# Kernel optimization log

Measured on AMD Instinct MI355X. Metric: run time of the kernel, lower is better.

Reference implementation:

```python
import jax, jax.numpy as jnp
import numpy as np

NUM_TASKS = 8
NUM_EXPERTS = 8
TOPK = 2
WEX = 0.01
N_TOKENS = 4194304


def setup_inputs() -> dict:
    key = jax.random.key(0)
    k1, k2 = jax.random.split(key)
    router_logits = jax.random.normal(k1, (N_TOKENS, NUM_EXPERTS), dtype=jnp.float32)
    router_labels = jax.random.randint(k2, (N_TOKENS,), 0, NUM_TASKS, dtype=jnp.int64)
    return {"router_logits": router_logits, "router_labels": router_labels}


def reference(router_logits, router_labels):
    # call_update: detached softmax over experts
    probs = jax.lax.stop_gradient(
        jax.nn.softmax(router_logits.astype(jnp.float32), axis=-1)
    )  # [N, E]
    labels = router_labels.astype(jnp.int32)
    # Torch loop `for task in router_labels` adds segment_sum[task] once per
    # occurrence of task -> EX_task_gate[t] = count[t] * segment_sum[t]
    seg_sum = jax.ops.segment_sum(probs, labels, num_segments=NUM_TASKS)  # [T, E]
    counts = jax.ops.segment_sum(
        jnp.ones((probs.shape[0],), dtype=jnp.float32), labels, num_segments=NUM_TASKS
    )  # [T]
    EX_gate = seg_sum * counts[:, None]  # [T, E]
    # calculate_mutual_information_loss
    tot = EX_gate.sum() / TOPK
    EX_gate = EX_gate / (tot + 0.0001)
    P_TI = EX_gate.sum(axis=1, keepdims=True) + 0.0001  # [T, 1]
    P_EI = EX_gate.sum(axis=0, keepdims=True) + 0.0001  # [1, E]
    expert_loss = -(EX_gate * jnp.log(EX_gate / P_TI / P_EI + 0.0001)).sum()
    return jnp.float32(WEX) * expert_loss
```

## Files before the change

### kernel.cpp

```cpp
#include <hip/hip_runtime.h>
#include <hip/hip_bf16.h>

#define N_TOKENS    4194304
#define NUM_EXPERTS 8
#define NUM_TASKS   8
#define GRID        2048
#define BLOCK       256
#define NTHREADS    (GRID * BLOCK)
#define ITERS       (N_TOKENS * 2 / NTHREADS)
#define BATCH       4

__global__ __launch_bounds__(BLOCK) void mi_reduce_kernel(
    const float* __restrict__ logits,
    const int*   __restrict__ labels,
    float*       __restrict__ ws) {

  float acc[NUM_TASKS][4];
#pragma unroll
  for (int t = 0; t < NUM_TASKS; ++t)
#pragma unroll
    for (int e = 0; e < 4; ++e) acc[t][e] = 0.0f;

  const int u    = blockIdx.x * BLOCK + threadIdx.x;
  const int tok0 = u >> 1;
  const float4* __restrict__ lp = reinterpret_cast<const float4*>(logits);

#pragma unroll
  for (int kb = 0; kb < ITERS / BATCH; ++kb) {
    float4 v[BATCH];
    int   lab[BATCH];
#pragma unroll
    for (int j = 0; j < BATCH; ++j) {
      const int k = kb * BATCH + j;
      v[j]   = lp[(size_t)k * NTHREADS + u];
      lab[j] = labels[k * (NTHREADS / 2) + tok0];
    }
#pragma unroll
    for (int j = 0; j < BATCH; ++j) {
      float mx = fmaxf(fmaxf(v[j].x, v[j].y), fmaxf(v[j].z, v[j].w));
      mx = fmaxf(mx, __shfl_xor(mx, 1, 64));
      float p0 = __expf(v[j].x - mx);
      float p1 = __expf(v[j].y - mx);
      float p2 = __expf(v[j].z - mx);
      float p3 = __expf(v[j].w - mx);
      float s = (p0 + p1) + (p2 + p3);
      s += __shfl_xor(s, 1, 64);
      float r = __builtin_amdgcn_rcpf(s);
      p0 *= r; p1 *= r; p2 *= r; p3 *= r;
#pragma unroll
      for (int t = 0; t < NUM_TASKS; ++t) {
        float m = (lab[j] == t) ? 1.0f : 0.0f;
        acc[t][0] = fmaf(m, p0, acc[t][0]);
        acc[t][1] = fmaf(m, p1, acc[t][1]);
        acc[t][2] = fmaf(m, p2, acc[t][2]);
        acc[t][3] = fmaf(m, p3, acc[t][3]);
      }
    }
  }

#pragma unroll
  for (int t = 0; t < NUM_TASKS; ++t)
#pragma unroll
    for (int e = 0; e < 4; ++e) {
      float x = acc[t][e];
#pragma unroll
      for (int m = 2; m < 64; m <<= 1) x += __shfl_xor(x, m, 64);
      acc[t][e] = x;
    }

  __shared__ float sacc[64];
  if (threadIdx.x < 64) sacc[threadIdx.x] = 0.0f;
  __syncthreads();
  const int lane = threadIdx.x & 63;
  if (lane < 2) {
    const int eoff = lane * 4;
#pragma unroll
    for (int t = 0; t < NUM_TASKS; ++t)
#pragma unroll
      for (int e = 0; e < 4; ++e)
        atomicAdd(&sacc[t * NUM_EXPERTS + eoff + e], acc[t][e]);
  }
  __syncthreads();
  if (threadIdx.x < 64) atomicAdd(&ws[threadIdx.x], sacc[threadIdx.x]);
}

__global__ void mi_finalize_kernel(const float* __restrict__ ws,
                                   float* __restrict__ out) {
  int lane = threadIdx.x;

  float seg = ws[lane];

  float c = seg;
  c += __shfl_xor(c, 1, 64);
  c += __shfl_xor(c, 2, 64);
  c += __shfl_xor(c, 4, 64);

  float ex = seg * c;

  float s = ex;
#pragma unroll
  for (int m = 1; m < 64; m <<= 1) s += __shfl_xor(s, m, 64);
  float tot = s * 0.5f;
  ex = ex / (tot + 1e-4f);

  float pti = ex;
  pti += __shfl_xor(pti, 1, 64);
  pti += __shfl_xor(pti, 2, 64);
  pti += __shfl_xor(pti, 4, 64);
  pti += 1e-4f;

  float pei = ex;
  pei += __shfl_xor(pei, 8, 64);
  pei += __shfl_xor(pei, 16, 64);
  pei += __shfl_xor(pei, 32, 64);
  pei += 1e-4f;

  float term = -ex * logf(ex / pti / pei + 1e-4f);
#pragma unroll
  for (int m = 1; m < 64; m <<= 1) term += __shfl_xor(term, m, 64);

  if (lane == 0) out[0] = 0.01f * term;
}

extern "C" void kernel_launch(void* const* d_in, const int* in_sizes, int n_in,
                              void* d_out, int out_size, void* d_ws, size_t ws_size,
                              hipStream_t stream) {
  const float* logits = (const float*)d_in[0];
  const int*   labels = (const int*)d_in[1];
  float* out = (float*)d_out;
  float* ws  = (float*)d_ws;

  hipMemsetAsync(ws, 0, 64 * sizeof(float), stream);

  mi_reduce_kernel<<<GRID, BLOCK, 0, stream>>>(logits, labels, ws);
  mi_finalize_kernel<<<1, 64, 0, stream>>>(ws, out);
}
```

Measured before the change: 232.8 us.

## Halve grid, double-buffer loads, replace global atomics with per-block partials

Halves the grid so each thread handles 32 token-halves, processed in four batches of 8. Loads are double-buffered so the next batch is in flight while the current one is reduced. The global atomicAdd and the memset are replaced by per-block partial writes, which a 1024-thread finalize kernel sums. This removes atomic contention and the memset launch, at the cost of higher register pressure and a larger finalize reduction.

```diff
diff --git a/kernel.cpp b/kernel.cpp
--- a/kernel.cpp
+++ b/kernel.cpp
@@ -4,16 +4,16 @@
 #define N_TOKENS    4194304
 #define NUM_EXPERTS 8
 #define NUM_TASKS   8
-#define GRID        2048
+#define GRID        1024
 #define BLOCK       256
-#define NTHREADS    (GRID * BLOCK)
-#define ITERS       (N_TOKENS * 2 / NTHREADS)
-#define BATCH       4
+#define NTH         (GRID * BLOCK)
+#define HSLOTS      (N_TOKENS * 2 / NTH)
+#define PF          8
 
 __global__ __launch_bounds__(BLOCK) void mi_reduce_kernel(
     const float* __restrict__ logits,
     const int*   __restrict__ labels,
-    float*       __restrict__ ws) {
+    float*       __restrict__ partials) {
 
   float acc[NUM_TASKS][4];
 #pragma unroll
@@ -25,38 +25,53 @@
   const int tok0 = u >> 1;
   const float4* __restrict__ lp = reinterpret_cast<const float4*>(logits);
 
-#pragma unroll
-  for (int kb = 0; kb < ITERS / BATCH; ++kb) {
-    float4 v[BATCH];
-    int   lab[BATCH];
-#pragma unroll
-    for (int j = 0; j < BATCH; ++j) {
-      const int k = kb * BATCH + j;
-      v[j]   = lp[(size_t)k * NTHREADS + u];
-      lab[j] = labels[k * (NTHREADS / 2) + tok0];
-    }
-#pragma unroll
-    for (int j = 0; j < BATCH; ++j) {
-      float mx = fmaxf(fmaxf(v[j].x, v[j].y), fmaxf(v[j].z, v[j].w));
-      mx = fmaxf(mx, __shfl_xor(mx, 1, 64));
-      float p0 = __expf(v[j].x - mx);
-      float p1 = __expf(v[j].y - mx);
-      float p2 = __expf(v[j].z - mx);
-      float p3 = __expf(v[j].w - mx);
-      float s = (p0 + p1) + (p2 + p3);
-      s += __shfl_xor(s, 1, 64);
-      float r = __builtin_amdgcn_rcpf(s);
-      p0 *= r; p1 *= r; p2 *= r; p3 *= r;
-#pragma unroll
-      for (int t = 0; t < NUM_TASKS; ++t) {
-        float m = (lab[j] == t) ? 1.0f : 0.0f;
-        acc[t][0] = fmaf(m, p0, acc[t][0]);
-        acc[t][1] = fmaf(m, p1, acc[t][1]);
-        acc[t][2] = fmaf(m, p2, acc[t][2]);
-        acc[t][3] = fmaf(m, p3, acc[t][3]);
-      }
-    }
+  float4 va[PF]; int la[PF];
+  float4 vb[PF]; int lb[PF];
+
+#define LOADB(ARR, LARR, B)                                                  \
+  _Pragma("unroll")                                                          \
+  for (int j = 0; j < PF; ++j) {                                             \
+    const int k = (B) * PF + j;                                              \
+    (ARR)[j]  = lp[(size_t)k * NTH + u];            \
+    (LARR)[j] = labels[k * (NTH / 2) + tok0];               \
   }
+
+#define PROC(ARR, LARR)                                                      \
+  _Pragma("unroll")                                                          \
+  for (int j = 0; j < PF; ++j) {                                             \
+    float4 w = (ARR)[j];                                                     \
+    float mx = fmaxf(fmaxf(w.x, w.y), fmaxf(w.z, w.w));                      \
+    mx = fmaxf(mx, __shfl_xor(mx, 1, 64));                                   \
+    float p0 = __expf(w.x - mx);                                             \
+    float p1 = __expf(w.y - mx);                                             \
+    float p2 = __expf(w.z - mx);                                             \
+    float p3 = __expf(w.w - mx);                                             \
+    float s = (p0 + p1) + (p2 + p3);                                         \
+    s += __shfl_xor(s, 1, 64);                                               \
+    float r = __builtin_amdgcn_rcpf(s);                                      \
+    p0 *= r; p1 *= r; p2 *= r; p3 *= r;                                      \
+    const int lab = (LARR)[j];                                               \
+    _Pragma("unroll")                                                        \
+    for (int t = 0; t < NUM_TASKS; ++t) {                                    \
+      float m = (lab == t) ? 1.0f : 0.0f;                                    \
+      acc[t][0] = fmaf(m, p0, acc[t][0]);                                    \
+      acc[t][1] = fmaf(m, p1, acc[t][1]);                                    \
+      acc[t][2] = fmaf(m, p2, acc[t][2]);                                    \
+      acc[t][3] = fmaf(m, p3, acc[t][3]);                                    \
+    }                                                                        \
+  }
+
+  LOADB(va, la, 0);
+  LOADB(vb, lb, 1);
+  PROC(va, la);
+  LOADB(va, la, 2);
+  PROC(vb, lb);
+  LOADB(vb, lb, 3);
+  PROC(va, la);
+  PROC(vb, lb);
+
+#undef LOADB
+#undef PROC
 
 #pragma unroll
   for (int t = 0; t < NUM_TASKS; ++t)
@@ -81,45 +96,66 @@
         atomicAdd(&sacc[t * NUM_EXPERTS + eoff + e], acc[t][e]);
   }
   __syncthreads();
-  if (threadIdx.x < 64) atomicAdd(&ws[threadIdx.x], sacc[threadIdx.x]);
+  if (threadIdx.x < 64)
+    partials[blockIdx.x * 64 + threadIdx.x] = sacc[threadIdx.x];
 }
 
-__global__ void mi_finalize_kernel(const float* __restrict__ ws,
-                                   float* __restrict__ out) {
-  int lane = threadIdx.x;
+__global__ __launch_bounds__(1024) void mi_finalize_kernel(
+    const float* __restrict__ partials,
+    float*       __restrict__ out) {
+  __shared__ float red[1024];
+  const int tid = threadIdx.x;
+  const int c   = tid & 63;
+  const int rb  = tid >> 6;
 
-  float seg = ws[lane];
+  float s = 0.0f;
+#pragma unroll
+  for (int r = rb; r < GRID; r += 16) s += partials[r * 64 + c];
+  red[tid] = s;
+  __syncthreads();
+  if (tid < 512) red[tid] += red[tid + 512];
+  __syncthreads();
+  if (tid < 256) red[tid] += red[tid + 256];
+  __syncthreads();
+  if (tid < 128) red[tid] += red[tid + 128];
+  __syncthreads();
+  if (tid < 64)  red[tid] += red[tid + 64];
+  __syncthreads();
 
-  float c = seg;
-  c += __shfl_xor(c, 1, 64);
-  c += __shfl_xor(c, 2, 64);
-  c += __shfl_xor(c, 4, 64);
+  if (tid < 64) {
+    float seg = red[tid];
 
-  float ex = seg * c;
+    float cnt = seg;
+    cnt += __shfl_xor(cnt, 1, 64);
+    cnt += __shfl_xor(cnt, 2, 64);
+    cnt += __shfl_xor(cnt, 4, 64);
 
-  float s = ex;
+    float ex = seg * cnt;
+
+    float tot = ex;
 #pragma unroll
-  for (int m = 1; m < 64; m <<= 1) s += __shfl_xor(s, m, 64);
-  float tot = s * 0.5f;
-  ex = ex / (tot + 1e-4f);
+    for (int m = 1; m < 64; m <<= 1) tot += __shfl_xor(tot, m, 64);
+    tot *= 0.5f;
+    ex = ex / (tot + 1e-4f);
 
-  float pti = ex;
-  pti += __shfl_xor(pti, 1, 64);
-  pti += __shfl_xor(pti, 2, 64);
-  pti += __shfl_xor(pti, 4, 64);
-  pti += 1e-4f;
+    float pti = ex;
+    pti += __shfl_xor(pti, 1, 64);
+    pti += __shfl_xor(pti, 2, 64);
+    pti += __shfl_xor(pti, 4, 64);
+    pti += 1e-4f;
 
-  float pei = ex;
-  pei += __shfl_xor(pei, 8, 64);
-  pei += __shfl_xor(pei, 16, 64);
-  pei += __shfl_xor(pei, 32, 64);
-  pei += 1e-4f;
+    float pei = ex;
+    pei += __shfl_xor(pei, 8, 64);
+    pei += __shfl_xor(pei, 16, 64);
+    pei += __shfl_xor(pei, 32, 64);
+    pei += 1e-4f;
 
-  float term = -ex * logf(ex / pti / pei + 1e-4f);
+    float term = -ex * logf(ex / pti / pei + 1e-4f);
 #pragma unroll
-  for (int m = 1; m < 64; m <<= 1) term += __shfl_xor(term, m, 64);
+    for (int m = 1; m < 64; m <<= 1) term += __shfl_xor(term, m, 64);
 
-  if (lane == 0) out[0] = 0.01f * term;
+    if (tid == 0) out[0] = 0.01f * term;
+  }
 }
 
 extern "C" void kernel_launch(void* const* d_in, const int* in_sizes, int n_in,
@@ -128,10 +164,8 @@
   const float* logits = (const float*)d_in[0];
   const int*   labels = (const int*)d_in[1];
   float* out = (float*)d_out;
-  float* ws  = (float*)d_ws;
+  float* partials = (float*)d_ws;
 
-  hipMemsetAsync(ws, 0, 64 * sizeof(float), stream);
-
-  mi_reduce_kernel<<<GRID, BLOCK, 0, stream>>>(logits, labels, ws);
-  mi_finalize_kernel<<<1, 64, 0, stream>>>(ws, out);
+  mi_reduce_kernel<<<GRID, BLOCK, 0, stream>>>(logits, labels, partials);
+  mi_finalize_kernel<<<1, 1024, 0, stream>>>(partials, out);
 }
```

After: 222.1 us. 1.05x faster.
